# Kernel tuning notes

Measured on AMD Instinct MI355X. Metric: run time of the kernel, lower is better.

Reference implementation:

```python
import jax, jax.numpy as jnp
import numpy as np

# dims
B, V, IMG = 16, 2, 224
G, PATCH, SG = 7, 14, 16
D, NH, L = 768, 12, 12
DH = D // NH            # 64
P = DH // 4             # rope frequencies per axis (2D axial RoPE)
N = G * G               # 49 glimpse tokens
S = SG * SG             # 256 scene tokens
GSIZE = G * PATCH       # 98 px glimpse


def _ln(x, w, b):
    m = x.mean(-1, keepdims=True)
    v = ((x - m) ** 2).mean(-1, keepdims=True)
    return (x - m) * jax.lax.rsqrt(v + 1e-6) * w + b


def _rope(pos, periods):
    # pos [B,N,2] -> cos,sin [B,N,2P]  (x freqs then y freqs)
    ang = (pos[..., :, None] / periods).reshape(pos.shape[0], pos.shape[1], -1)
    return jnp.cos(ang), jnp.sin(ang)


def _apply_rope(x, cos, sin):
    # x [B,H,N,DH]; cos/sin [B,N,DH//2]
    c = cos[:, None, :, :]
    s = sin[:, None, :, :]
    xr = x.reshape(x.shape[0], x.shape[1], x.shape[2], DH // 2, 2)
    x1, x2 = xr[..., 0], xr[..., 1]
    return jnp.stack([x1 * c - x2 * s, x1 * s + x2 * c], -1).reshape(x.shape)


def _heads(x):
    return x.reshape(x.shape[0], x.shape[1], NH, DH).transpose(0, 2, 1, 3)


def _merge(x):
    return x.transpose(0, 2, 1, 3).reshape(x.shape[0], x.shape[2], D)


def _attn(q, k, v):
    a = jax.nn.softmax(jnp.einsum('bhqd,bhkd->bhqk', q, k) / jnp.sqrt(jnp.float32(DH)), axis=-1)
    return jnp.einsum('bhqk,bhkd->bhqd', a, v)


def _cross(xq, xkv, qw, qb, kvw, kvb, ow, ob, rq, rkv):
    q = _heads(xq @ qw.T + qb)
    kv = xkv @ kvw.T + kvb
    k, v = _heads(kv[..., :D]), _heads(kv[..., D:])
    q = _apply_rope(q, *rq)
    k = _apply_rope(k, *rkv)
    return _merge(_attn(q, k, v)) @ ow.T + ob


def _bilinear(img, py, px):
    # img [C,H,W], py/px [GSIZE] pixel coords -> [C,GSIZE,GSIZE]
    Hh, Ww = img.shape[1], img.shape[2]
    y0 = jnp.clip(jnp.floor(py), 0, Hh - 2).astype(jnp.int32)
    x0 = jnp.clip(jnp.floor(px), 0, Ww - 2).astype(jnp.int32)
    wy = jnp.clip(py - y0, 0.0, 1.0)[None, :, None]
    wx = jnp.clip(px - x0, 0.0, 1.0)[None, None, :]
    g0, g1 = img[:, y0, :], img[:, y0 + 1, :]
    v00, v01 = g0[:, :, x0], g0[:, :, x0 + 1]
    v10, v11 = g1[:, :, x0], g1[:, :, x0 + 1]
    return (v00 * (1 - wy) + v10 * wy) * (1 - wx) + (v01 * (1 - wy) + v11 * wy) * wx


def _extract(images, c, s):
    # crop a [-1,1]-normalized glimpse of half-width `scale` at `center`
    lin = jnp.linspace(-1.0, 1.0, GSIZE)
    gy = c[:, 1:2] + s[:, None] * lin
    gx = c[:, 0:1] + s[:, None] * lin
    py = (gy + 1.0) * 0.5 * (images.shape[2] - 1)
    px = (gx + 1.0) * 0.5 * (images.shape[3] - 1)
    return jax.vmap(_bilinear)(images, py, px)


def _forward(images, centers, scales, patch_w, patch_b, scene_tokens,
             ln1_w, ln1_b, ln2_w, ln2_b, qkv_w, qkv_b, attn_out_w, attn_out_b,
             mlp_w1, mlp_b1, mlp_w2, mlp_b2,
             read_q_w, read_q_b, read_kv_w, read_kv_b, read_out_w, read_out_b, read_gate,
             write_q_w, write_q_b, write_kv_w, write_kv_b, write_out_w, write_out_b, write_gate):
    periods = 100.0 ** (jnp.arange(P, dtype=jnp.float32) / P)
    lin_s = jnp.linspace(-1.0, 1.0, SG)
    ys, xs = jnp.meshgrid(lin_s, lin_s, indexing='ij')
    scene_pos = jnp.broadcast_to(jnp.stack([xs.ravel(), ys.ravel()], -1), (B, S, 2))
    scene_rope = _rope(scene_pos, periods)
    lin_g = jnp.linspace(-1.0, 1.0, G)
    yg, xg = jnp.meshgrid(lin_g, lin_g, indexing='ij')
    goffs = jnp.stack([xg.ravel(), yg.ravel()], -1)  # [N,2]

    scene = jnp.broadcast_to(scene_tokens, (B, S, D))
    for vp in range(V):
        glimpse = _extract(images, centers[vp], scales[vp])  # [B,3,98,98]
        t = jax.lax.conv_general_dilated(glimpse, patch_w, (PATCH, PATCH), 'VALID',
                                         dimension_numbers=('NCHW', 'OIHW', 'NCHW'))
        local = t.reshape(B, D, N).transpose(0, 2, 1) + patch_b  # [B,49,D]
        lpos = centers[vp][:, None, :] + scales[vp][:, None, None] * goffs
        lrope = _rope(lpos, periods)
        for i in range(L):
            local = local + read_gate[i] * _cross(local, scene,
                read_q_w[i], read_q_b[i], read_kv_w[i], read_kv_b[i],
                read_out_w[i], read_out_b[i], lrope, scene_rope)
            # ViT block with RoPE self-attention
            h = _ln(local, ln1_w[i], ln1_b[i])
            qkv = h @ qkv_w[i].T + qkv_b[i]
            q, k, v = _heads(qkv[..., :D]), _heads(qkv[..., D:2 * D]), _heads(qkv[..., 2 * D:])
            q = _apply_rope(q, *lrope)
            k = _apply_rope(k, *lrope)
            local = local + _merge(_attn(q, k, v)) @ attn_out_w[i].T + attn_out_b[i]
            h = _ln(local, ln2_w[i], ln2_b[i])
            local = local + jax.nn.gelu(h @ mlp_w1[i].T + mlp_b1[i]) @ mlp_w2[i].T + mlp_b2[i]
            scene = scene + write_gate[i] * _cross(scene, local,
                write_q_w[i], write_q_b[i], write_kv_w[i], write_kv_b[i],
                write_out_w[i], write_out_b[i], scene_rope, lrope)
    return scene  # [B,S,D]


def setup_inputs() -> dict:
    key = jax.random.key(0)
    ks = iter(jax.random.split(key, 40))
    std = 0.02
    d = {}
    d['images'] = jax.random.normal(next(ks), (B, 3, IMG, IMG), jnp.float32)
    d['centers'] = jax.random.uniform(next(ks), (V, B, 2), jnp.float32, -0.5, 0.5)
    d['scales'] = jax.random.uniform(next(ks), (V, B), jnp.float32, 0.2, 0.4)
    d['patch_w'] = jax.random.normal(next(ks), (D, 3, PATCH, PATCH), jnp.float32) * std
    d['patch_b'] = jnp.zeros((D,), jnp.float32)
    d['scene_tokens'] = jax.random.normal(next(ks), (1, S, D), jnp.float32) / jnp.sqrt(jnp.float32(D))
    d['ln1_w'] = jnp.ones((L, D), jnp.float32); d['ln1_b'] = jnp.zeros((L, D), jnp.float32)
    d['ln2_w'] = jnp.ones((L, D), jnp.float32); d['ln2_b'] = jnp.zeros((L, D), jnp.float32)
    d['qkv_w'] = jax.random.normal(next(ks), (L, 3 * D, D), jnp.float32) * std
    d['qkv_b'] = jnp.zeros((L, 3 * D), jnp.float32)
    d['attn_out_w'] = jax.random.normal(next(ks), (L, D, D), jnp.float32) * std
    d['attn_out_b'] = jnp.zeros((L, D), jnp.float32)
    d['mlp_w1'] = jax.random.normal(next(ks), (L, 4 * D, D), jnp.float32) * std
    d['mlp_b1'] = jnp.zeros((L, 4 * D), jnp.float32)
    d['mlp_w2'] = jax.random.normal(next(ks), (L, D, 4 * D), jnp.float32) * std
    d['mlp_b2'] = jnp.zeros((L, D), jnp.float32)
    for pre in ('read', 'write'):
        d[pre + '_q_w'] = jax.random.normal(next(ks), (L, D, D), jnp.float32) * std
        d[pre + '_q_b'] = jnp.zeros((L, D), jnp.float32)
        d[pre + '_kv_w'] = jax.random.normal(next(ks), (L, 2 * D, D), jnp.float32) * std
        d[pre + '_kv_b'] = jnp.zeros((L, 2 * D), jnp.float32)
        d[pre + '_out_w'] = jax.random.normal(next(ks), (L, D, D), jnp.float32) * std
        d[pre + '_out_b'] = jnp.zeros((L, D), jnp.float32)
        d[pre + '_gate'] = jax.random.normal(next(ks), (L, D), jnp.float32) * 0.1
    return d


def reference(images, centers, scales, patch_w, patch_b, scene_tokens,
              ln1_w, ln1_b, ln2_w, ln2_b, qkv_w, qkv_b, attn_out_w, attn_out_b,
              mlp_w1, mlp_b1, mlp_w2, mlp_b2,
              read_q_w, read_q_b, read_kv_w, read_kv_b, read_out_w, read_out_b, read_gate,
              write_q_w, write_q_b, write_kv_w, write_kv_b, write_out_w, write_out_b, write_gate):
    return _forward(images, centers, scales, patch_w, patch_b, scene_tokens,
                    ln1_w, ln1_b, ln2_w, ln2_b, qkv_w, qkv_b, attn_out_w, attn_out_b,
                    mlp_w1, mlp_b1, mlp_w2, mlp_b2,
                    read_q_w, read_q_b, read_kv_w, read_kv_b, read_out_w, read_out_b, read_gate,
                    write_q_w, write_q_b, write_kv_w, write_kv_b, write_out_w, write_out_b, write_gate)
```

## Files before the change

kernel.cpp:

```cpp
#include <hip/hip_runtime.h>

#define B_ 16
#define V_ 2
#define D_ 768
#define NH_ 12
#define L_ 12
#define DH_ 64
#define N_ 49
#define S_ 256

__device__ __forceinline__ unsigned short f2bf(float f) {
  unsigned int u = __builtin_bit_cast(unsigned int, f);
  u += 0x7fffu + ((u >> 16) & 1u);
  return (unsigned short)(u >> 16);
}
__device__ __forceinline__ float bf2f(unsigned short h) {
  unsigned int u = ((unsigned int)h) << 16;
  return __builtin_bit_cast(float, u);
}
__device__ __forceinline__ float bflo(unsigned int w) {
  return __builtin_bit_cast(float, w << 16);
}
__device__ __forceinline__ float bfhi(unsigned int w) {
  return __builtin_bit_cast(float, w & 0xffff0000u);
}
__device__ __forceinline__ unsigned int packbf2(float a, float b) {
  return (unsigned int)f2bf(a) | ((unsigned int)f2bf(b) << 16);
}

using bf16x8 = __attribute__((ext_vector_type(8))) __bf16;
using u16x8  = __attribute__((ext_vector_type(8))) unsigned short;
using f32x4  = __attribute__((ext_vector_type(4))) float;

__device__ __forceinline__ void g2l16(const unsigned short* g, unsigned short* l) {
  __builtin_amdgcn_global_load_lds(
      (const __attribute__((address_space(1))) unsigned int*)g,
      (__attribute__((address_space(3))) unsigned int*)l, 16, 0, 0);
}

template <int BM, int BN, int BK, bool SWZ>
__global__ __launch_bounds__(256) void gemm_v6(
    const unsigned short* __restrict__ A, int lda,
    const unsigned short* __restrict__ W, int ldw,
    const float* __restrict__ bias,
    float* __restrict__ Cf, unsigned short* __restrict__ Cb, int ldc,
    const float* __restrict__ res, const float* __restrict__ gate,
    int M, int N, int K, int epi)
{
  __shared__ unsigned short As[2][BM * BK];
  __shared__ unsigned short Bs[2][BN * BK];
  constexpr int FM = BM / 32, FN = BN / 32;
  constexpr int CPR = BK / 8;
  constexpr int LPS = (BM + BN) * BK / 2048;
  int m0, n0;
  if (SWZ) {
    const int gx = gridDim.x;
    const int nwg = gx * gridDim.y;
    const int orig = blockIdx.y * gx + blockIdx.x;
    const int xcd = orig & 7, rem = orig >> 3;
    const int qq = nwg >> 3, rr = nwg & 7;
    const int wgid = (xcd < rr ? xcd * (qq + 1) : rr * (qq + 1) + (xcd - rr) * qq) + rem;
    m0 = (wgid % gx) * BM; n0 = (wgid / gx) * BN;
  } else {
    m0 = blockIdx.x * BM; n0 = blockIdx.y * BN;
  }
  const int tid = threadIdx.x, lane = tid & 63, wid = tid >> 6;
  const int wr = wid >> 1, wc = wid & 1;
  const int fr = lane & 15, kq8 = lane >> 4;

  f32x4 acc[FM][FN];
#pragma unroll
  for (int mi = 0; mi < FM; ++mi)
#pragma unroll
    for (int ni = 0; ni < FN; ++ni) acc[mi][ni] = f32x4{0.f, 0.f, 0.f, 0.f};

  auto stage = [&](int buf, int k0) {
    const unsigned short* Ab = A + (size_t)m0 * lda + k0;
    const unsigned short* Bb = W + (size_t)n0 * ldw + k0;
#pragma unroll
    for (int ra = 0; ra < BM * BK / 2048; ++ra) {
      int c = ra * 256 + tid;
      int row = c / CPR, slot = c % CPR;
      int gslot = slot ^ (row & 7);
      g2l16(Ab + (size_t)row * lda + gslot * 8, &As[buf][c * 8]);
    }
#pragma unroll
    for (int rb = 0; rb < BN * BK / 2048; ++rb) {
      int c = rb * 256 + tid;
      int row = c / CPR, slot = c % CPR;
      int gslot = slot ^ (row & 7);
      g2l16(Bb + (size_t)row * ldw + gslot * 8, &Bs[buf][c * 8]);
    }
  };

  const int nt = K / BK;
  stage(0, 0);
  int cur = 0;
  for (int t = 0; t < nt; ++t) {
    if (t + 1 < nt) {
      stage(cur ^ 1, (t + 1) * BK);
      asm volatile("s_waitcnt vmcnt(%0)" :: "i"(LPS) : "memory");
    } else {
      asm volatile("s_waitcnt vmcnt(0)" ::: "memory");
    }
    __builtin_amdgcn_s_barrier();
#pragma unroll
    for (int ks = 0; ks < BK / 32; ++ks) {
      bf16x8 av[FM], bv[FN];
#pragma unroll
      for (int mi = 0; mi < FM; ++mi) {
        int row = wr * (BM / 2) + mi * 16 + fr;
        int idx = row * BK + (((ks * 4 + kq8) ^ (row & 7)) << 3);
        av[mi] = __builtin_bit_cast(bf16x8, *(const u16x8*)&As[cur][idx]);
      }
#pragma unroll
      for (int ni = 0; ni < FN; ++ni) {
        int row = wc * (BN / 2) + ni * 16 + fr;
        int idx = row * BK + (((ks * 4 + kq8) ^ (row & 7)) << 3);
        bv[ni] = __builtin_bit_cast(bf16x8, *(const u16x8*)&Bs[cur][idx]);
      }
#pragma unroll
      for (int mi = 0; mi < FM; ++mi)
#pragma unroll
        for (int ni = 0; ni < FN; ++ni)
          acc[mi][ni] = __builtin_amdgcn_mfma_f32_16x16x32_bf16(av[mi], bv[ni], acc[mi][ni], 0, 0, 0);
    }
    __builtin_amdgcn_s_barrier();
    cur ^= 1;
  }

  const int er = (lane >> 4) * 4, ec = lane & 15;
#pragma unroll
  for (int mi = 0; mi < FM; ++mi)
#pragma unroll
    for (int ni = 0; ni < FN; ++ni) {
      int gc = n0 + wc * (BN / 2) + ni * 16 + ec;
      float bi = bias ? bias[gc] : 0.0f;
      float gg = gate ? gate[gc] : 1.0f;
#pragma unroll
      for (int i = 0; i < 4; ++i) {
        int gr = m0 + wr * (BM / 2) + mi * 16 + er + i;
        if (gr < M) {
          float v = acc[mi][ni][i] + bi;
          if (epi == 1) {
            v = v / (1.0f + __expf(-1.59576912f * (v + 0.044715f * v * v * v)));
          } else if (epi == 2) {
            v = res[(size_t)gr * ldc + gc] + gg * v;
          }
          if (Cf) Cf[(size_t)gr * ldc + gc] = v;
          if (Cb) Cb[(size_t)gr * ldc + gc] = f2bf(v);
        }
      }
    }
}

template <int LKPAD>
__global__ __launch_bounds__(256) void attn_mfma(
    const unsigned short* __restrict__ Q, int ldq, int qoff, int Lq,
    const unsigned short* __restrict__ KV, int ldkv, int koff, int voff, int Lk,
    const float* __restrict__ cq, const float* __restrict__ sq, int rbq,
    const float* __restrict__ ck, const float* __restrict__ sk, int rbk,
    unsigned short* __restrict__ Out)
{
  constexpr int NT = LKPAD / 16;
  constexpr int NKS = LKPAD / 32;
  __shared__ unsigned short Kb[LKPAD * 64];
  __shared__ unsigned short Vt[64 * LKPAD];
  __shared__ unsigned short Qs[4][16 * 64];
  __shared__ unsigned short Pl[4][16 * LKPAD];
  const int b = blockIdx.x / NH_, h = blockIdx.x - b * NH_;
  const int tid = threadIdx.x, lane = tid & 63, wid = tid >> 6;

  for (int idx = tid; idx < LKPAD * 32; idx += 256) {
    int t = idx >> 5, m = idx & 31;
    int d = 2 * m;
    int ksl = (t << 6) + (((m >> 2) ^ (t & 7)) << 3) + ((m & 3) << 1);
    int vs0 = d * LKPAD + (((t >> 3) ^ (d & 7)) << 3) + (t & 7);
    int vs1 = (d + 1) * LKPAD + (((t >> 3) ^ ((d + 1) & 7)) << 3) + (t & 7);
    if (t < Lk) {
      size_t rowb = ((size_t)b * Lk + t) * ldkv;
      unsigned int kw = *(const unsigned int*)(KV + rowb + koff + h * DH_ + d);
      unsigned int vw = *(const unsigned int*)(KV + rowb + voff + h * DH_ + d);
      float k1 = bflo(kw), k2 = bfhi(kw);
      size_t ri = (size_t)b * rbk + (size_t)t * 32 + m;
      float c = ck[ri], s = sk[ri];
      *(unsigned int*)&Kb[ksl] = packbf2((k1 * c - k2 * s) * 0.125f, (k1 * s + k2 * c) * 0.125f);
      Vt[vs0] = (unsigned short)(vw & 0xffff);
      Vt[vs1] = (unsigned short)(vw >> 16);
    } else {
      *(unsigned int*)&Kb[ksl] = 0;
      Vt[vs0] = 0; Vt[vs1] = 0;
    }
  }
  const int qbase = blockIdx.y * 64 + wid * 16;
  for (int idx = lane; idx < 16 * 32; idx += 64) {
    int r = idx >> 5, m = idx & 31;
    int gq = qbase + r;
    unsigned int qr = 0;
    if (gq < Lq) {
      unsigned int qw = *(const unsigned int*)(Q + ((size_t)b * Lq + gq) * ldq + qoff + h * DH_ + 2 * m);
      float q1 = bflo(qw), q2 = bfhi(qw);
      size_t ri = (size_t)b * rbq + (size_t)gq * 32 + m;
      float c = cq[ri], s = sq[ri];
      qr = packbf2(q1 * c - q2 * s, q1 * s + q2 * c);
    }
    *(unsigned int*)&Qs[wid][(r << 6) + (((m >> 2) ^ (r & 7)) << 3) + ((m & 3) << 1)] = qr;
  }
  __syncthreads();

  const int fr = lane & 15, g = lane >> 4;
  bf16x8 qa[2];
#pragma unroll
  for (int ks = 0; ks < 2; ++ks)
    qa[ks] = __builtin_bit_cast(bf16x8,
        *(const u16x8*)&Qs[wid][(fr << 6) + ((((ks << 2) + g) ^ (fr & 7)) << 3)]);

  f32x4 sv[NT];
  __builtin_amdgcn_s_setprio(1);
#pragma unroll
  for (int t = 0; t < NT; ++t) {
    int key = (t << 4) + fr;
    f32x4 a = {0.f, 0.f, 0.f, 0.f};
#pragma unroll
    for (int ks = 0; ks < 2; ++ks) {
      bf16x8 kb = __builtin_bit_cast(bf16x8,
          *(const u16x8*)&Kb[(key << 6) + ((((ks << 2) + g) ^ (key & 7)) << 3)]);
      a = __builtin_amdgcn_mfma_f32_16x16x32_bf16(qa[ks], kb, a, 0, 0, 0);
    }
    sv[t] = a;
  }
  __builtin_amdgcn_s_setprio(0);
#pragma unroll
  for (int t = 0; t < NT; ++t) {
    int key = (t << 4) + fr;
    if (key >= Lk) sv[t] = f32x4{-1e30f, -1e30f, -1e30f, -1e30f};
  }
  f32x4 mx = sv[0];
#pragma unroll
  for (int t = 1; t < NT; ++t)
#pragma unroll
    for (int i = 0; i < 4; ++i) mx[i] = fmaxf(mx[i], sv[t][i]);
#pragma unroll
  for (int off = 1; off <= 8; off <<= 1)
#pragma unroll
    for (int i = 0; i < 4; ++i) mx[i] = fmaxf(mx[i], __shfl_xor(mx[i], off));
  f32x4 sm = {0.f, 0.f, 0.f, 0.f};
#pragma unroll
  for (int t = 0; t < NT; ++t)
#pragma unroll
    for (int i = 0; i < 4; ++i) {
      float e = __expf(sv[t][i] - mx[i]);
      sv[t][i] = e;
      sm[i] += e;
    }
#pragma unroll
  for (int off = 1; off <= 8; off <<= 1)
#pragma unroll
    for (int i = 0; i < 4; ++i) sm[i] += __shfl_xor(sm[i], off);
  f32x4 inv;
#pragma unroll
  for (int i = 0; i < 4; ++i) inv[i] = 1.0f / sm[i];
#pragma unroll
  for (int t = 0; t < NT; ++t) {
    int key = (t << 4) + fr;
    int chunk = key >> 3;
#pragma unroll
    for (int i = 0; i < 4; ++i) {
      int row = (g << 2) + i;
      Pl[wid][row * LKPAD + ((chunk ^ (row & 7)) << 3) + (key & 7)] = f2bf(sv[t][i]);
    }
  }
  f32x4 oacc[4];
#pragma unroll
  for (int n = 0; n < 4; ++n) oacc[n] = f32x4{0.f, 0.f, 0.f, 0.f};
  __builtin_amdgcn_s_setprio(1);
#pragma unroll
  for (int ks = 0; ks < NKS; ++ks) {
    int chunk = (ks << 2) + g;
    bf16x8 pa = __builtin_bit_cast(bf16x8,
        *(const u16x8*)&Pl[wid][fr * LKPAD + ((chunk ^ (fr & 7)) << 3)]);
#pragma unroll
    for (int n = 0; n < 4; ++n) {
      int drow = (n << 4) + fr;
      bf16x8 vb = __builtin_bit_cast(bf16x8,
          *(const u16x8*)&Vt[drow * LKPAD + ((chunk ^ (drow & 7)) << 3)]);
      oacc[n] = __builtin_amdgcn_mfma_f32_16x16x32_bf16(pa, vb, oacc[n], 0, 0, 0);
    }
  }
  __builtin_amdgcn_s_setprio(0);
#pragma unroll
  for (int n = 0; n < 4; ++n)
#pragma unroll
    for (int i = 0; i < 4; ++i) {
      int gq = qbase + (g << 2) + i;
      if (gq < Lq)
        Out[((size_t)b * Lq + gq) * D_ + h * DH_ + (n << 4) + fr] = f2bf(oacc[n][i] * inv[i]);
    }
}

__global__ __launch_bounds__(256) void ln_kernel(
    const float* __restrict__ X, const float* __restrict__ w,
    const float* __restrict__ bsh, unsigned short* __restrict__ Out)
{
  const int row = blockIdx.x, tid = threadIdx.x;
  const float* x = X + (size_t)row * D_;
  float v0 = x[tid], v1 = x[tid + 256], v2 = x[tid + 512];
  __shared__ float red[4];
  float s = v0 + v1 + v2;
  for (int o = 32; o; o >>= 1) s += __shfl_xor(s, o);
  if ((tid & 63) == 0) red[tid >> 6] = s;
  __syncthreads();
  float mean = (red[0] + red[1] + red[2] + red[3]) * (1.0f / 768.0f);
  float d0 = v0 - mean, d1 = v1 - mean, d2 = v2 - mean;
  float q = d0 * d0 + d1 * d1 + d2 * d2;
  __syncthreads();
  for (int o = 32; o; o >>= 1) q += __shfl_xor(q, o);
  if ((tid & 63) == 0) red[tid >> 6] = q;
  __syncthreads();
  float var = (red[0] + red[1] + red[2] + red[3]) * (1.0f / 768.0f);
  float rstd = rsqrtf(var + 1e-6f);
  Out[(size_t)row * D_ + tid]       = f2bf(d0 * rstd * w[tid]       + bsh[tid]);
  Out[(size_t)row * D_ + tid + 256] = f2bf(d1 * rstd * w[tid + 256] + bsh[tid + 256]);
  Out[(size_t)row * D_ + tid + 512] = f2bf(d2 * rstd * w[tid + 512] + bsh[tid + 512]);
}

struct CvtA {
  const float* s[11];
  unsigned short* d[11];
  unsigned int lsrc[11];
  unsigned int lstride[11];
  int blkEnd[11];
};
__global__ __launch_bounds__(256) void cvt_multi_k(CvtA c) {
  int bid = blockIdx.x;
  int seg = 0;
#pragma unroll
  for (int i = 0; i < 10; ++i) seg += (bid >= c.blkEnd[i]) ? 1 : 0;
  unsigned int e = (unsigned int)(bid - (seg ? c.blkEnd[seg - 1] : 0)) * 2048u
                   + (unsigned int)threadIdx.x * 8u;
  unsigned int l = e / c.lsrc[seg], r = e - l * c.lsrc[seg];
  const float* s = c.s[seg] + e;
  unsigned short* d = c.d[seg] + (size_t)l * c.lstride[seg] + r;
  f32x4 a = *(const f32x4*)s, b2 = *(const f32x4*)(s + 4);
  u16x8 o;
  o[0] = f2bf(a.x); o[1] = f2bf(a.y); o[2] = f2bf(a.z); o[3] = f2bf(a.w);
  o[4] = f2bf(b2.x); o[5] = f2bf(b2.y); o[6] = f2bf(b2.z); o[7] = f2bf(b2.w);
  *(u16x8*)d = o;
}

__global__ void cvt_patch_k(const float* __restrict__ s, unsigned short* __restrict__ d) {
  int i = blockIdx.x * 256 + threadIdx.x;
  if (i >= 768 * 768) return;
  int r = i / 768, col = i - r * 768;
  d[i] = f2bf(col < 588 ? s[r * 588 + col] : 0.0f);
}

__global__ void fbias_k(const float* __restrict__ wqb, const float* __restrict__ rkvb,
                        float* __restrict__ fb) {
  int i = blockIdx.x * 256 + threadIdx.x;
  if (i >= L_ * 2304) return;
  int l = i / 2304, c = i - l * 2304;
  fb[i] = (c < 768) ? wqb[l * 768 + c] : rkvb[l * 1536 + (c - 768)];
}

__global__ void fbias2_k(const float* __restrict__ wkvb, const float* __restrict__ rqb,
                         float* __restrict__ fb2) {
  int i = blockIdx.x * 256 + threadIdx.x;
  if (i >= L_ * 2304) return;
  int l = i / 2304, c = i - l * 2304;
  fb2[i] = (c < 1536) ? wkvb[l * 1536 + c] : rqb[((l + 1) % L_) * 768 + (c - 1536)];
}

__global__ void init_scene_k(const float* __restrict__ tok, float* __restrict__ sf,
                             unsigned short* __restrict__ sb, int total) {
  int i = blockIdx.x * 256 + threadIdx.x;
  if (i < total) {
    float v = tok[i % (S_ * D_)];
    sf[i] = v; sb[i] = f2bf(v);
  }
}

__global__ void rope_scene_k(float* __restrict__ c, float* __restrict__ s) {
  int idx = blockIdx.x * 256 + threadIdx.x;
  if (idx >= S_ * 32) return;
  int t = idx >> 5, m = idx & 31;
  int i = t >> 4, j = t & 15;
  float xx = -1.0f + 2.0f * j / 15.0f;
  float yy = -1.0f + 2.0f * i / 15.0f;
  float coord = (m < 16) ? xx : yy;
  float per = powf(100.0f, (float)(m & 15) / 16.0f);
  float ang = coord / per;
  c[idx] = cosf(ang); s[idx] = sinf(ang);
}

__global__ void rope_local_k(float* __restrict__ c, float* __restrict__ s,
                             const float* __restrict__ ctr, const float* __restrict__ scl) {
  int idx = blockIdx.x * 256 + threadIdx.x;
  if (idx >= B_ * N_ * 32) return;
  int b = idx / (N_ * 32);
  int r = idx - b * (N_ * 32);
  int pch = r >> 5, m = r & 31;
  int py = pch / 7, px = pch - py * 7;
  float cx = ctr[b * 2], cy = ctr[b * 2 + 1], sc = scl[b];
  float gx = cx + sc * ((px - 3.0f) / 3.0f);
  float gy = cy + sc * ((py - 3.0f) / 3.0f);
  float coord = (m < 16) ? gx : gy;
  float per = powf(100.0f, (float)(m & 15) / 16.0f);
  float ang = coord / per;
  c[idx] = cosf(ang); s[idx] = sinf(ang);
}

__global__ void im2col_k(unsigned short* __restrict__ xb, const float* __restrict__ img,
                         const float* __restrict__ ctr, const float* __restrict__ scl) {
  int idx = blockIdx.x * 256 + threadIdx.x;
  if (idx >= 784 * 768) return;
  int row = idx / 768, col = idx - row * 768;
  float val = 0.0f;
  if (col < 588) {
    int b = row / 49, pch = row - b * 49;
    int c = col / 196, rr = col - c * 196;
    int i = rr / 14, j = rr - i * 14;
    int py = pch / 7, px = pch - py * 7;
    int gyi = py * 14 + i, gxi = px * 14 + j;
    float cx = ctr[b * 2], cy = ctr[b * 2 + 1], sc = scl[b];
    float gy = cy + sc * (-1.0f + 2.0f * gyi / 97.0f);
    float gx = cx + sc * (-1.0f + 2.0f * gxi / 97.0f);
    float pyi = (gy + 1.0f) * 0.5f * 223.0f;
    float pxi = (gx + 1.0f) * 0.5f * 223.0f;
    float y0f = fminf(fmaxf(floorf(pyi), 0.0f), 222.0f);
    float x0f = fminf(fmaxf(floorf(pxi), 0.0f), 222.0f);
    int y0 = (int)y0f, x0 = (int)x0f;
    float wy = fminf(fmaxf(pyi - y0f, 0.0f), 1.0f);
    float wx = fminf(fmaxf(pxi - x0f, 0.0f), 1.0f);
    const float* base = img + (size_t)(b * 3 + c) * 224 * 224;
    float v00 = base[y0 * 224 + x0],       v01 = base[y0 * 224 + x0 + 1];
    float v10 = base[(y0 + 1) * 224 + x0], v11 = base[(y0 + 1) * 224 + x0 + 1];
    val = (v00 * (1.0f - wy) + v10 * wy) * (1.0f - wx) + (v01 * (1.0f - wy) + v11 * wy) * wx;
  }
  xb[idx] = f2bf(val);
}

extern "C" void kernel_launch(void* const* d_in, const int* in_sizes, int n_in,
                              void* d_out, int out_size, void* d_ws, size_t ws_size,
                              hipStream_t stream) {
  const float* images    = (const float*)d_in[0];
  const float* centers   = (const float*)d_in[1];
  const float* scales    = (const float*)d_in[2];
  const float* patch_w   = (const float*)d_in[3];
  const float* patch_b   = (const float*)d_in[4];
  const float* scene_tok = (const float*)d_in[5];
  const float* ln1_w = (const float*)d_in[6];
  const float* ln1_b = (const float*)d_in[7];
  const float* ln2_w = (const float*)d_in[8];
  const float* ln2_b = (const float*)d_in[9];
  const float* qkv_w = (const float*)d_in[10];
  const float* qkv_b = (const float*)d_in[11];
  const float* ao_w  = (const float*)d_in[12];
  const float* ao_b  = (const float*)d_in[13];
  const float* m1_w  = (const float*)d_in[14];
  const float* m1_b  = (const float*)d_in[15];
  const float* m2_w  = (const float*)d_in[16];
  const float* m2_b  = (const float*)d_in[17];
  const float* rq_w  = (const float*)d_in[18];
  const float* rq_b  = (const float*)d_in[19];
  const float* rkv_w = (const float*)d_in[20];
  const float* rkv_b = (const float*)d_in[21];
  const float* ro_w  = (const float*)d_in[22];
  const float* ro_b  = (const float*)d_in[23];
  const float* rgate = (const float*)d_in[24];
  const float* wq_w  = (const float*)d_in[25];
  const float* wq_b  = (const float*)d_in[26];
  const float* wkv_w = (const float*)d_in[27];
  const float* wkv_b = (const float*)d_in[28];
  const float* wo_w  = (const float*)d_in[29];
  const float* wo_b  = (const float*)d_in[30];
  const float* wgate = (const float*)d_in[31];

  float* scene_f = (float*)d_out;

  char* p = (char*)d_ws;
  auto alloc = [&](size_t bytes) { char* r = p; p += (bytes + 255) & ~(size_t)255; return (void*)r; };
  unsigned short* scene_bf = (unsigned short*)alloc((size_t)4096 * 768 * 2);
  float*          local_f  = (float*)alloc((size_t)784 * 768 * 4);
  unsigned short* local_bf = (unsigned short*)alloc((size_t)896 * 768 * 2);
  unsigned short* q_r_bf   = (unsigned short*)alloc((size_t)896 * 768 * 2);
  unsigned short* qrkv_bf  = (unsigned short*)alloc((size_t)4096 * 2304 * 2);
  unsigned short* kv_bf    = (unsigned short*)alloc((size_t)896 * 2304 * 2);
  unsigned short* kvq_bf   = (unsigned short*)alloc((size_t)896 * 2304 * 2);
  unsigned short* ln_bf    = (unsigned short*)alloc((size_t)896 * 768 * 2);
  unsigned short* act_bf   = (unsigned short*)alloc((size_t)4096 * 768 * 2);
  unsigned short* x_bf     = (unsigned short*)alloc((size_t)896 * 768 * 2);
  float* sc_cos = (float*)alloc((size_t)S_ * 32 * 4);
  float* sc_sin = (float*)alloc((size_t)S_ * 32 * 4);
  float* l_cos  = (float*)alloc((size_t)B_ * N_ * 32 * 4);
  float* l_sin  = (float*)alloc((size_t)B_ * N_ * 32 * 4);
  unsigned short* patch_wbf = (unsigned short*)alloc((size_t)768 * 768 * 2);
  float*          fb        = (float*)alloc((size_t)L_ * 2304 * 4);
  float*          fb2       = (float*)alloc((size_t)L_ * 2304 * 4);

  static const size_t REGSZ[9] = {589824, 1769472, 589824, 1769472, 589824,
                                  2359296, 2359296, 1769472, 589824};
  struct SegDef { const float* src; int reg; unsigned off; unsigned lsrc; int nl; };
  const SegDef SEGS[11] = {
    {rq_w,            0, 0,       589824,  L_},
    {wq_w,            1, 0,       589824,  L_},
    {rkv_w,           1, 589824,  1179648, L_},
    {ro_w,            2, 0,       589824,  L_},
    {qkv_w,           3, 0,       1769472, L_},
    {ao_w,            4, 0,       589824,  L_},
    {m1_w,            5, 0,       2359296, L_},
    {m2_w,            6, 0,       2359296, L_},
    {wkv_w,           7, 0,       1179648, L_},
    {rq_w + 589824,   7, 1179648, 589824,  L_ - 1},
    {wo_w,            8, 0,       589824,  L_},
  };
  size_t regBase[9];
  size_t perLayer = 0;
  {
    size_t cur = 0;
    for (int i = 0; i < 9; ++i) { regBase[i] = cur; cur += REGSZ[i] * L_; perLayer += REGSZ[i]; }
  }
  const size_t allElems = perLayer * L_;
  size_t usedBytes = (size_t)(p - (char*)d_ws);
  bool preconv = ws_size >= usedBytes + allElems * 2 + 4096;
  unsigned short* wbf = (unsigned short*)alloc((preconv ? allElems : perLayer) * 2);

  auto GQ = [&](const unsigned short* A, int lda, const unsigned short* Wp,
                const float* bias, float* Cf, unsigned short* Cb, int ldc,
                const float* res, const float* gt, int N, int epi) {
    gemm_v6<128, 128, 64, true><<<dim3(32, N / 128), 256, 0, stream>>>(
        A, lda, Wp, 768, bias, Cf, Cb, ldc, res, gt, 4096, N, 768, epi);
  };
  auto GW = [&](const unsigned short* A, int lda, const unsigned short* Wp,
                const float* bias, float* Cf, unsigned short* Cb, int ldc,
                const float* res, const float* gt, int N, int epi) {
    gemm_v6<128, 64, 64, true><<<dim3(32, N / 64), 256, 0, stream>>>(
        A, lda, Wp, 768, bias, Cf, Cb, ldc, res, gt, 4096, N, 768, epi);
  };
  auto GS = [&](const unsigned short* A, int lda, const unsigned short* Wp, int ldw,
                const float* bias, float* Cf, unsigned short* Cb, int ldc,
                const float* res, const float* gt, int N, int K, int epi) {
    gemm_v6<64, 64, 128, false><<<dim3(13, N / 64), 256, 0, stream>>>(
        A, lda, Wp, ldw, bias, Cf, Cb, ldc, res, gt, 784, N, K, epi);
  };

  {
    int total = B_ * S_ * D_;
    init_scene_k<<<(total + 255) / 256, 256, 0, stream>>>(scene_tok, scene_f, scene_bf, total);
    rope_scene_k<<<(S_ * 32 + 255) / 256, 256, 0, stream>>>(sc_cos, sc_sin);
    cvt_patch_k<<<(768 * 768 + 255) / 256, 256, 0, stream>>>(patch_w, patch_wbf);
    fbias_k<<<(L_ * 2304 + 255) / 256, 256, 0, stream>>>(wq_b, rkv_b, fb);
    fbias2_k<<<(L_ * 2304 + 255) / 256, 256, 0, stream>>>(wkv_b, rq_b, fb2);
    if (preconv) {
      CvtA cv;
      int blk = 0;
      for (int i = 0; i < 11; ++i) {
        cv.s[i] = SEGS[i].src;
        cv.d[i] = wbf + regBase[SEGS[i].reg] + SEGS[i].off;
        cv.lsrc[i] = SEGS[i].lsrc;
        cv.lstride[i] = (unsigned)REGSZ[SEGS[i].reg];
        blk += (int)((size_t)SEGS[i].lsrc * SEGS[i].nl / 2048);
        cv.blkEnd[i] = blk;
      }
      cvt_multi_k<<<blk, 256, 0, stream>>>(cv);
    }
  }

  for (int vp = 0; vp < V_; ++vp) {
    const float* ctr = centers + (size_t)vp * B_ * 2;
    const float* scl = scales + (size_t)vp * B_;
    rope_local_k<<<(B_ * N_ * 32 + 255) / 256, 256, 0, stream>>>(l_cos, l_sin, ctr, scl);
    im2col_k<<<(784 * 768 + 255) / 256, 256, 0, stream>>>(x_bf, images, ctr, scl);
    GS(x_bf, 768, patch_wbf, 768, patch_b, local_f, local_bf, 768,
       nullptr, nullptr, 768, 768, 0);

    for (int l = 0; l < L_; ++l) {
      const unsigned short* wR[9];
      if (preconv) {
        for (int rg = 0; rg < 9; ++rg)
          wR[rg] = wbf + regBase[rg] + (size_t)l * REGSZ[rg];
      } else {
        CvtA cv;
        int blk = 0;
        size_t cur = 0;
        size_t rb[9];
        for (int rg = 0; rg < 9; ++rg) { rb[rg] = cur; cur += REGSZ[rg]; wR[rg] = wbf + rb[rg]; }
        for (int i = 0; i < 11; ++i) {
          size_t srcl = (i == 9) ? (size_t)((l + 1) % L_) : (size_t)l;
          cv.s[i] = (i == 9 ? rq_w : SEGS[i].src) + srcl * SEGS[i].lsrc;
          cv.d[i] = wbf + rb[SEGS[i].reg] + SEGS[i].off;
          cv.lsrc[i] = SEGS[i].lsrc;
          cv.lstride[i] = (unsigned)REGSZ[SEGS[i].reg];
          blk += (int)(SEGS[i].lsrc / 2048);
          cv.blkEnd[i] = blk;
        }
        cvt_multi_k<<<blk, 256, 0, stream>>>(cv);
      }

      GQ(scene_bf, 768, wR[1], fb + (size_t)l * 2304,
         nullptr, qrkv_bf, 2304, nullptr, nullptr, 2304, 0);
      if (l == 0)
        GS(local_bf, 768, wR[0], 768, rq_b + l * 768,
           nullptr, q_r_bf, 768, nullptr, nullptr, 768, 768, 0);
      if (l == 0)
        attn_mfma<256><<<dim3(B_ * NH_, 1), 256, 0, stream>>>(q_r_bf, 768, 0, 49,
            qrkv_bf, 2304, 768, 1536, 256, l_cos, l_sin, N_ * 32, sc_cos, sc_sin, 0, act_bf);
      else
        attn_mfma<256><<<dim3(B_ * NH_, 1), 256, 0, stream>>>(kvq_bf, 2304, 1536, 49,
            qrkv_bf, 2304, 768, 1536, 256, l_cos, l_sin, N_ * 32, sc_cos, sc_sin, 0, act_bf);
      GS(act_bf, 768, wR[2], 768, ro_b + l * 768,
         local_f, local_bf, 768, local_f, rgate + l * 768, 768, 768, 2);
      ln_kernel<<<784, 256, 0, stream>>>(local_f, ln1_w + l * 768, ln1_b + l * 768, ln_bf);
      GS(ln_bf, 768, wR[3], 768, qkv_b + (size_t)l * 2304,
         nullptr, kv_bf, 2304, nullptr, nullptr, 2304, 768, 0);
      attn_mfma<64><<<dim3(B_ * NH_, 1), 256, 0, stream>>>(kv_bf, 2304, 0, 49,
          kv_bf, 2304, 768, 1536, 49, l_cos, l_sin, N_ * 32, l_cos, l_sin, N_ * 32, act_bf);
      GS(act_bf, 768, wR[4], 768, ao_b + l * 768,
         local_f, local_bf, 768, local_f, nullptr, 768, 768, 2);
      ln_kernel<<<784, 256, 0, stream>>>(local_f, ln2_w + l * 768, ln2_b + l * 768, ln_bf);
      GS(ln_bf, 768, wR[5], 768, m1_b + (size_t)l * 3072,
         nullptr, act_bf, 3072, nullptr, nullptr, 3072, 768, 1);
      GS(act_bf, 3072, wR[6], 3072, m2_b + l * 768,
         local_f, local_bf, 768, local_f, nullptr, 768, 3072, 2);
      GS(local_bf, 768, wR[7], 768, fb2 + (size_t)l * 2304,
         nullptr, kvq_bf, 2304, nullptr, nullptr, 2304, 768, 0);
      attn_mfma<64><<<dim3(B_ * NH_, 4), 256, 0, stream>>>(qrkv_bf, 2304, 0, 256,
          kvq_bf, 2304, 0, 768, 49, sc_cos, sc_sin, 0, l_cos, l_sin, N_ * 32, act_bf);
      GW(act_bf, 768, wR[8], wo_b + l * 768,
         scene_f, scene_bf, 768, scene_f, wgate + l * 768, 768, 2);
    }
  }
}
```

Measured before the change: 6.271 ms.

## Fold LayerNorm into following GEMMs using residual-epilogue row statistics

Removes the two standalone LayerNorm kernels per layer. The LN gamma is folded into the QKV and MLP1 weights during bf16 conversion, and a precomputed column sum and beta-folded bias are applied in the GEMM epilogue. The per-row sum and sum of squares are accumulated with atomics in the preceding residual GEMM epilogue. This saves a launch and a full pass over the activations twice per layer, but the GEMM now reads the un-normalised bf16 residual, and the variance computed as E[x²]−mean² in fp32 can lose precision. It also adds atomics and a restructured epilogue loop.

New measurement: 6.919 ms. +10.3%, slower.

```diff
diff --git a/kernel.cpp b/kernel.cpp
--- a/kernel.cpp
+++ b/kernel.cpp
@@ -39,12 +39,13 @@
 }
 
 template <int BM, int BN, int BK, bool SWZ>
-__global__ __launch_bounds__(256) void gemm_v6(
+__global__ __launch_bounds__(256) void gemm_v7(
     const unsigned short* __restrict__ A, int lda,
     const unsigned short* __restrict__ W, int ldw,
     const float* __restrict__ bias,
     float* __restrict__ Cf, unsigned short* __restrict__ Cb, int ldc,
     const float* __restrict__ res, const float* __restrict__ gate,
+    float* __restrict__ stats,
     int M, int N, int K, int epi)
 {
   __shared__ unsigned short As[2][BM * BK];
@@ -131,27 +132,55 @@
 
   const int er = (lane >> 4) * 4, ec = lane & 15;
 #pragma unroll
-  for (int mi = 0; mi < FM; ++mi)
-#pragma unroll
-    for (int ni = 0; ni < FN; ++ni) {
-      int gc = n0 + wc * (BN / 2) + ni * 16 + ec;
-      float bi = bias ? bias[gc] : 0.0f;
-      float gg = gate ? gate[gc] : 1.0f;
-#pragma unroll
-      for (int i = 0; i < 4; ++i) {
-        int gr = m0 + wr * (BM / 2) + mi * 16 + er + i;
+  for (int mi = 0; mi < FM; ++mi) {
+#pragma unroll
+    for (int i = 0; i < 4; ++i) {
+      int gr = m0 + wr * (BM / 2) + mi * 16 + er + i;
+      float mu = 0.f, rs = 0.f;
+      if (epi >= 3) {
+        float su = stats[gr * 2], sq = stats[gr * 2 + 1];
+        mu = su * (1.0f / 768.0f);
+        rs = rsqrtf(fmaxf(sq * (1.0f / 768.0f) - mu * mu, 0.f) + 1e-6f);
+      }
+      float s = 0.f, q = 0.f;
+#pragma unroll
+      for (int ni = 0; ni < FN; ++ni) {
+        int gc = n0 + wc * (BN / 2) + ni * 16 + ec;
+        float bi = bias ? bias[gc] : 0.0f;
+        float gg = gate ? gate[gc] : 1.0f;
+        float v = acc[mi][ni][i];
+        if (epi == 0) {
+          v += bi;
+        } else if (epi == 1) {
+          v += bi;
+          v = v / (1.0f + __expf(-1.59576912f * (v + 0.044715f * v * v * v)));
+        } else if (epi == 2) {
+          v += bi;
+          if (gr < M) v = res[(size_t)gr * ldc + gc] + gg * v;
+        } else {
+          v = (v - mu * gg) * rs + bi;
+          if (epi == 4)
+            v = v / (1.0f + __expf(-1.59576912f * (v + 0.044715f * v * v * v)));
+        }
         if (gr < M) {
-          float v = acc[mi][ni][i] + bi;
-          if (epi == 1) {
-            v = v / (1.0f + __expf(-1.59576912f * (v + 0.044715f * v * v * v)));
-          } else if (epi == 2) {
-            v = res[(size_t)gr * ldc + gc] + gg * v;
-          }
           if (Cf) Cf[(size_t)gr * ldc + gc] = v;
           if (Cb) Cb[(size_t)gr * ldc + gc] = f2bf(v);
         }
+        s += v; q += v * v;
       }
-    }
+      if (epi == 2 && stats) {
+#pragma unroll
+        for (int off = 1; off <= 8; off <<= 1) {
+          s += __shfl_xor(s, off);
+          q += __shfl_xor(q, off);
+        }
+        if ((lane & 15) == 0 && gr < M) {
+          atomicAdd(&stats[gr * 2], s);
+          atomicAdd(&stats[gr * 2 + 1], q);
+        }
+      }
+    }
+  }
 }
 
 template <int LKPAD>
@@ -298,35 +327,10 @@
     }
 }
 
-__global__ __launch_bounds__(256) void ln_kernel(
-    const float* __restrict__ X, const float* __restrict__ w,
-    const float* __restrict__ bsh, unsigned short* __restrict__ Out)
-{
-  const int row = blockIdx.x, tid = threadIdx.x;
-  const float* x = X + (size_t)row * D_;
-  float v0 = x[tid], v1 = x[tid + 256], v2 = x[tid + 512];
-  __shared__ float red[4];
-  float s = v0 + v1 + v2;
-  for (int o = 32; o; o >>= 1) s += __shfl_xor(s, o);
-  if ((tid & 63) == 0) red[tid >> 6] = s;
-  __syncthreads();
-  float mean = (red[0] + red[1] + red[2] + red[3]) * (1.0f / 768.0f);
-  float d0 = v0 - mean, d1 = v1 - mean, d2 = v2 - mean;
-  float q = d0 * d0 + d1 * d1 + d2 * d2;
-  __syncthreads();
-  for (int o = 32; o; o >>= 1) q += __shfl_xor(q, o);
-  if ((tid & 63) == 0) red[tid >> 6] = q;
-  __syncthreads();
-  float var = (red[0] + red[1] + red[2] + red[3]) * (1.0f / 768.0f);
-  float rstd = rsqrtf(var + 1e-6f);
-  Out[(size_t)row * D_ + tid]       = f2bf(d0 * rstd * w[tid]       + bsh[tid]);
-  Out[(size_t)row * D_ + tid + 256] = f2bf(d1 * rstd * w[tid + 256] + bsh[tid + 256]);
-  Out[(size_t)row * D_ + tid + 512] = f2bf(d2 * rstd * w[tid + 512] + bsh[tid + 512]);
-}
-
 struct CvtA {
   const float* s[11];
   unsigned short* d[11];
+  const float* g[11];
   unsigned int lsrc[11];
   unsigned int lstride[11];
   int blkEnd[11];
@@ -342,10 +346,54 @@
   const float* s = c.s[seg] + e;
   unsigned short* d = c.d[seg] + (size_t)l * c.lstride[seg] + r;
   f32x4 a = *(const f32x4*)s, b2 = *(const f32x4*)(s + 4);
+  const float* gp = c.g[seg];
+  if (gp) {
+    unsigned int k = e % 768u;
+    const float* gpp = gp + (size_t)l * 768u + k;
+    f32x4 ga = *(const f32x4*)gpp, gb = *(const f32x4*)(gpp + 4);
+    a.x *= ga.x; a.y *= ga.y; a.z *= ga.z; a.w *= ga.w;
+    b2.x *= gb.x; b2.y *= gb.y; b2.z *= gb.z; b2.w *= gb.w;
+  }
   u16x8 o;
   o[0] = f2bf(a.x); o[1] = f2bf(a.y); o[2] = f2bf(a.z); o[3] = f2bf(a.w);
   o[4] = f2bf(b2.x); o[5] = f2bf(b2.y); o[6] = f2bf(b2.z); o[7] = f2bf(b2.w);
   *(u16x8*)d = o;
+}
+
+__global__ __launch_bounds__(256) void foldprep_k(
+    const float* __restrict__ qkvw, const float* __restrict__ qkvb,
+    const float* __restrict__ g1, const float* __restrict__ b1,
+    const float* __restrict__ m1w, const float* __restrict__ m1b,
+    const float* __restrict__ g2, const float* __restrict__ b2,
+    float* __restrict__ cq, float* __restrict__ bq,
+    float* __restrict__ cm, float* __restrict__ bm)
+{
+  int row = blockIdx.x * 4 + (threadIdx.x >> 6);
+  int lane = threadIdx.x & 63;
+  const int QT = L_ * 2304;
+  const float *wrow, *gv, *bv;
+  float bb; float *co, *bo; int oi;
+  if (row < QT) {
+    int l = row / 2304, n = row - l * 2304;
+    wrow = qkvw + ((size_t)l * 2304 + n) * 768;
+    gv = g1 + l * 768; bv = b1 + l * 768;
+    bb = qkvb[row]; co = cq; bo = bq; oi = row;
+  } else {
+    int r2 = row - QT;
+    int l = r2 / 3072, n = r2 - l * 3072;
+    wrow = m1w + ((size_t)l * 3072 + n) * 768;
+    gv = g2 + l * 768; bv = b2 + l * 768;
+    bb = m1b[r2]; co = cm; bo = bm; oi = r2;
+  }
+  float cs = 0.f, bs = 0.f;
+#pragma unroll
+  for (int j = 0; j < 12; ++j) {
+    float w = wrow[lane + 64 * j];
+    cs += w * gv[lane + 64 * j];
+    bs += w * bv[lane + 64 * j];
+  }
+  for (int o = 32; o; o >>= 1) { cs += __shfl_xor(cs, o); bs += __shfl_xor(bs, o); }
+  if (lane == 0) { co[oi] = cs; bo[oi] = bb + bs; }
 }
 
 __global__ void cvt_patch_k(const float* __restrict__ s, unsigned short* __restrict__ d) {
@@ -487,7 +535,6 @@
   unsigned short* qrkv_bf  = (unsigned short*)alloc((size_t)4096 * 2304 * 2);
   unsigned short* kv_bf    = (unsigned short*)alloc((size_t)896 * 2304 * 2);
   unsigned short* kvq_bf   = (unsigned short*)alloc((size_t)896 * 2304 * 2);
-  unsigned short* ln_bf    = (unsigned short*)alloc((size_t)896 * 768 * 2);
   unsigned short* act_bf   = (unsigned short*)alloc((size_t)4096 * 768 * 2);
   unsigned short* x_bf     = (unsigned short*)alloc((size_t)896 * 768 * 2);
   float* sc_cos = (float*)alloc((size_t)S_ * 32 * 4);
@@ -497,22 +544,28 @@
   unsigned short* patch_wbf = (unsigned short*)alloc((size_t)768 * 768 * 2);
   float*          fb        = (float*)alloc((size_t)L_ * 2304 * 4);
   float*          fb2       = (float*)alloc((size_t)L_ * 2304 * 4);
+  float*          cq_v      = (float*)alloc((size_t)L_ * 2304 * 4);
+  float*          bq_v      = (float*)alloc((size_t)L_ * 2304 * 4);
+  float*          cm_v      = (float*)alloc((size_t)L_ * 3072 * 4);
+  float*          bm_v      = (float*)alloc((size_t)L_ * 3072 * 4);
+  const size_t ST_SLICE = 896 * 2;
+  float*          statsAll  = (float*)alloc((size_t)V_ * L_ * 2 * ST_SLICE * 4);
 
   static const size_t REGSZ[9] = {589824, 1769472, 589824, 1769472, 589824,
                                   2359296, 2359296, 1769472, 589824};
-  struct SegDef { const float* src; int reg; unsigned off; unsigned lsrc; int nl; };
+  struct SegDef { const float* src; int reg; unsigned off; unsigned lsrc; int nl; const float* gma; };
   const SegDef SEGS[11] = {
-    {rq_w,            0, 0,       589824,  L_},
-    {wq_w,            1, 0,       589824,  L_},
-    {rkv_w,           1, 589824,  1179648, L_},
-    {ro_w,            2, 0,       589824,  L_},
-    {qkv_w,           3, 0,       1769472, L_},
-    {ao_w,            4, 0,       589824,  L_},
-    {m1_w,            5, 0,       2359296, L_},
-    {m2_w,            6, 0,       2359296, L_},
-    {wkv_w,           7, 0,       1179648, L_},
-    {rq_w + 589824,   7, 1179648, 589824,  L_ - 1},
-    {wo_w,            8, 0,       589824,  L_},
+    {rq_w,            0, 0,       589824,  L_,    nullptr},
+    {wq_w,            1, 0,       589824,  L_,    nullptr},
+    {rkv_w,           1, 589824,  1179648, L_,    nullptr},
+    {ro_w,            2, 0,       589824,  L_,    nullptr},
+    {qkv_w,           3, 0,       1769472, L_,    ln1_w},
+    {ao_w,            4, 0,       589824,  L_,    nullptr},
+    {m1_w,            5, 0,       2359296, L_,    ln2_w},
+    {m2_w,            6, 0,       2359296, L_,    nullptr},
+    {wkv_w,           7, 0,       1179648, L_,    nullptr},
+    {rq_w + 589824,   7, 1179648, 589824,  L_ - 1, nullptr},
+    {wo_w,            8, 0,       589824,  L_,    nullptr},
   };
   size_t regBase[9];
   size_t perLayer = 0;
@@ -528,35 +581,39 @@
   auto GQ = [&](const unsigned short* A, int lda, const unsigned short* Wp,
                 const float* bias, float* Cf, unsigned short* Cb, int ldc,
                 const float* res, const float* gt, int N, int epi) {
-    gemm_v6<128, 128, 64, true><<<dim3(32, N / 128), 256, 0, stream>>>(
-        A, lda, Wp, 768, bias, Cf, Cb, ldc, res, gt, 4096, N, 768, epi);
+    gemm_v7<128, 128, 64, true><<<dim3(32, N / 128), 256, 0, stream>>>(
+        A, lda, Wp, 768, bias, Cf, Cb, ldc, res, gt, nullptr, 4096, N, 768, epi);
   };
   auto GW = [&](const unsigned short* A, int lda, const unsigned short* Wp,
                 const float* bias, float* Cf, unsigned short* Cb, int ldc,
                 const float* res, const float* gt, int N, int epi) {
-    gemm_v6<128, 64, 64, true><<<dim3(32, N / 64), 256, 0, stream>>>(
-        A, lda, Wp, 768, bias, Cf, Cb, ldc, res, gt, 4096, N, 768, epi);
+    gemm_v7<128, 64, 64, true><<<dim3(32, N / 64), 256, 0, stream>>>(
+        A, lda, Wp, 768, bias, Cf, Cb, ldc, res, gt, nullptr, 4096, N, 768, epi);
   };
   auto GS = [&](const unsigned short* A, int lda, const unsigned short* Wp, int ldw,
                 const float* bias, float* Cf, unsigned short* Cb, int ldc,
-                const float* res, const float* gt, int N, int K, int epi) {
-    gemm_v6<64, 64, 128, false><<<dim3(13, N / 64), 256, 0, stream>>>(
-        A, lda, Wp, ldw, bias, Cf, Cb, ldc, res, gt, 784, N, K, epi);
+                const float* res, const float* gt, float* st, int N, int K, int epi) {
+    gemm_v7<64, 64, 128, false><<<dim3(13, N / 64), 256, 0, stream>>>(
+        A, lda, Wp, ldw, bias, Cf, Cb, ldc, res, gt, st, 784, N, K, epi);
   };
 
   {
+    hipMemsetAsync(statsAll, 0, (size_t)V_ * L_ * 2 * ST_SLICE * 4, stream);
     int total = B_ * S_ * D_;
     init_scene_k<<<(total + 255) / 256, 256, 0, stream>>>(scene_tok, scene_f, scene_bf, total);
     rope_scene_k<<<(S_ * 32 + 255) / 256, 256, 0, stream>>>(sc_cos, sc_sin);
     cvt_patch_k<<<(768 * 768 + 255) / 256, 256, 0, stream>>>(patch_w, patch_wbf);
     fbias_k<<<(L_ * 2304 + 255) / 256, 256, 0, stream>>>(wq_b, rkv_b, fb);
     fbias2_k<<<(L_ * 2304 + 255) / 256, 256, 0, stream>>>(wkv_b, rq_b, fb2);
+    foldprep_k<<<(L_ * (2304 + 3072)) / 4, 256, 0, stream>>>(
+        qkv_w, qkv_b, ln1_w, ln1_b, m1_w, m1_b, ln2_w, ln2_b, cq_v, bq_v, cm_v, bm_v);
     if (preconv) {
       CvtA cv;
       int blk = 0;
       for (int i = 0; i < 11; ++i) {
         cv.s[i] = SEGS[i].src;
         cv.d[i] = wbf + regBase[SEGS[i].reg] + SEGS[i].off;
+        cv.g[i] = SEGS[i].gma;
         cv.lsrc[i] = SEGS[i].lsrc;
         cv.lstride[i] = (unsigned)REGSZ[SEGS[i].reg];
         blk += (int)((size_t)SEGS[i].lsrc * SEGS[i].nl / 2048);
@@ -572,7 +629,7 @@
     rope_local_k<<<(B_ * N_ * 32 + 255) / 256, 256, 0, stream>>>(l_cos, l_sin, ctr, scl);
     im2col_k<<<(784 * 768 + 255) / 256, 256, 0, stream>>>(x_bf, images, ctr, scl);
     GS(x_bf, 768, patch_wbf, 768, patch_b, local_f, local_bf, 768,
-       nullptr, nullptr, 768, 768, 0);
+       nullptr, nullptr, nullptr, 768, 768, 0);
 
     for (int l = 0; l < L_; ++l) {
       const unsigned short* wR[9];
@@ -589,6 +646,7 @@
           size_t srcl = (i == 9) ? (size_t)((l + 1) % L_) : (size_t)l;
           cv.s[i] = (i == 9 ? rq_w : SEGS[i].src) + srcl * SEGS[i].lsrc;
           cv.d[i] = wbf + rb[SEGS[i].reg] + SEGS[i].off;
+          cv.g[i] = SEGS[i].gma ? SEGS[i].gma + srcl * 768 : nullptr;
           cv.lsrc[i] = SEGS[i].lsrc;
           cv.lstride[i] = (unsigned)REGSZ[SEGS[i].reg];
           blk += (int)(SEGS[i].lsrc / 2048);
@@ -596,12 +654,14 @@
         }
         cvt_multi_k<<<blk, 256, 0, stream>>>(cv);
       }
+      float* stats1 = statsAll + ((size_t)(vp * L_ + l) * 2 + 0) * ST_SLICE;
+      float* stats2 = statsAll + ((size_t)(vp * L_ + l) * 2 + 1) * ST_SLICE;
 
       GQ(scene_bf, 768, wR[1], fb + (size_t)l * 2304,
          nullptr, qrkv_bf, 2304, nullptr, nullptr, 2304, 0);
       if (l == 0)
         GS(local_bf, 768, wR[0], 768, rq_b + l * 768,
-           nullptr, q_r_bf, 768, nullptr, nullptr, 768, 768, 0);
+           nullptr, q_r_bf, 768, nullptr, nullptr, nullptr, 768, 768, 0);
       if (l == 0)
         attn_mfma<256><<<dim3(B_ * NH_, 1), 256, 0, stream>>>(q_r_bf, 768, 0, 49,
             qrkv_bf, 2304, 768, 1536, 256, l_cos, l_sin, N_ * 32, sc_cos, sc_sin, 0, act_bf);
@@ -609,21 +669,19 @@
         attn_mfma<256><<<dim3(B_ * NH_, 1), 256, 0, stream>>>(kvq_bf, 2304, 1536, 49,
             qrkv_bf, 2304, 768, 1536, 256, l_cos, l_sin, N_ * 32, sc_cos, sc_sin, 0, act_bf);
       GS(act_bf, 768, wR[2], 768, ro_b + l * 768,
-         local_f, local_bf, 768, local_f, rgate + l * 768, 768, 768, 2);
-      ln_kernel<<<784, 256, 0, stream>>>(local_f, ln1_w + l * 768, ln1_b + l * 768, ln_bf);
-      GS(ln_bf, 768, wR[3], 768, qkv_b + (size_t)l * 2304,
-         nullptr, kv_bf, 2304, nullptr, nullptr, 2304, 768, 0);
+         local_f, local_bf, 768, local_f, rgate + l * 768, stats1, 768, 768, 2);
+      GS(local_bf, 768, wR[3], 768, bq_v + (size_t)l * 2304,
+         nullptr, kv_bf, 2304, nullptr, cq_v + (size_t)l * 2304, stats1, 2304, 768, 3);
       attn_mfma<64><<<dim3(B_ * NH_, 1), 256, 0, stream>>>(kv_bf, 2304, 0, 49,
           kv_bf, 2304, 768, 1536, 49, l_cos, l_sin, N_ * 32, l_cos, l_sin, N_ * 32, act_bf);
       GS(act_bf, 768, wR[4], 768, ao_b + l * 768,
-         local_f, local_bf, 768, local_f, nullptr, 768, 768, 2);
-      ln_kernel<<<784, 256, 0, stream>>>(local_f, ln2_w + l * 768, ln2_b + l * 768, ln_bf);
-      GS(ln_bf, 768, wR[5], 768, m1_b + (size_t)l * 3072,
-         nullptr, act_bf, 3072, nullptr, nullptr, 3072, 768, 1);
+         local_f, local_bf, 768, local_f, nullptr, stats2, 768, 768, 2);
+      GS(local_bf, 768, wR[5], 768, bm_v + (size_t)l * 3072,
+         nullptr, act_bf, 3072, nullptr, cm_v + (size_t)l * 3072, stats2, 3072, 768, 4);
       GS(act_bf, 3072, wR[6], 3072, m2_b + l * 768,
-         local_f, local_bf, 768, local_f, nullptr, 768, 3072, 2);
+         local_f, local_bf, 768, local_f, nullptr, nullptr, 768, 3072, 2);
       GS(local_bf, 768, wR[7], 768, fb2 + (size_t)l * 2304,
-         nullptr, kvq_bf, 2304, nullptr, nullptr, 2304, 768, 0);
+         nullptr, kvq_bf, 2304, nullptr, nullptr, nullptr, 2304, 768, 0);
       attn_mfma<64><<<dim3(B_ * NH_, 4), 256, 0, stream>>>(qrkv_bf, 2304, 0, 256,
           kvq_bf, 2304, 0, 768, 49, sc_cos, sc_sin, 0, l_cos, l_sin, N_ * 32, act_bf);
       GW(act_bf, 768, wR[8], wo_b + l * 768,
```
